# Kernel tuning notes

Hardware: AMD Instinct MI355X
Metric: run time of the kernel (lower is better)

The kernel has to match this reference:

```python
import jax, jax.numpy as jnp
import numpy as np

D_MODEL = 1024
D_STATE = 16
D_CONV = 4
LN_EPS = 1e-5


def setup_inputs() -> dict:
    key = jax.random.key(0)
    ks = jax.random.split(key, 12)
    B, T, D = 2, 2048, D_MODEL
    DI, DS, K = D_MODEL, D_STATE, D_CONV
    s = lambda k, shape, fan: jax.random.normal(k, shape, dtype=jnp.float32) * (1.0 / np.sqrt(fan))
    return {
        "x": jax.random.normal(ks[0], (B, T, D), dtype=jnp.float32),
        "ln_g": jnp.ones((D,), jnp.float32),
        "ln_b": jnp.zeros((D,), jnp.float32),
        "W_in": s(ks[1], (D, 2 * DI), D),          # x @ W_in -> [B,T,2*DI]
        "conv_w": s(ks[2], (DI, 1, K), K),          # depthwise conv kernel (OIH)
        "conv_b": jnp.zeros((DI,), jnp.float32),
        "dt_w": s(ks[3], (DI, DI), DI),
        "dt_b": jnp.zeros((DI,), jnp.float32),
        "B_w": s(ks[4], (DI, DS), DI),
        "C_w": s(ks[5], (DI, DS), DI),
        "log_A": jnp.log(jnp.linspace(1.0, 16.0, DI)).astype(jnp.float32),
        "D_param": jnp.ones((DI,), jnp.float32),
        "W_out": s(ks[6], (DI, D), DI),
    }


def _layernorm(x, g, b):
    mu = jnp.mean(x, axis=-1, keepdims=True)
    var = jnp.mean(jnp.square(x - mu), axis=-1, keepdims=True)
    return (x - mu) * jax.lax.rsqrt(var + LN_EPS) * g + b


def _causal_depthwise_conv(x, w, b):
    # x: [B,T,DI], w: [DI,1,K] -> causal conv, output [B,T,DI]
    xc = jnp.transpose(x, (0, 2, 1))  # [B,DI,T]
    K = w.shape[-1]
    out = jax.lax.conv_general_dilated(
        xc, w, window_strides=(1,), padding=[(K - 1, 0)],
        dimension_numbers=("NCH", "OIH", "NCH"),
        feature_group_count=x.shape[-1])
    return jnp.transpose(out, (0, 2, 1)) + b


def _ssm_scan(x, dt, Bm, Cm, A):
    # x, dt: [B,T,DI]; Bm, Cm: [B,T,DS]; A: [DI]
    Bsz, T, DI = x.shape
    DS = Bm.shape[-1]
    h0 = jnp.zeros((Bsz, DI, DS), jnp.float32)

    def step(h, inp):
        xt, dtt, bt, ct = inp  # [B,DI],[B,DI],[B,DS],[B,DS]
        decay = jnp.exp(jnp.minimum(dtt * A, 0.0))            # [B,DI]
        h = h * decay[..., None] + (dtt * xt)[..., None] * bt[:, None, :]
        y = jnp.einsum("bds,bs->bd", h, ct)
        return h, y

    xs = (jnp.swapaxes(x, 0, 1), jnp.swapaxes(dt, 0, 1),
          jnp.swapaxes(Bm, 0, 1), jnp.swapaxes(Cm, 0, 1))
    _, ys = jax.lax.scan(step, h0, xs)  # ys: [T,B,DI]
    return jnp.swapaxes(ys, 0, 1)


def reference(x, ln_g, ln_b, W_in, conv_w, conv_b, dt_w, dt_b, B_w, C_w, log_A, D_param, W_out):
    residual = x
    xn = _layernorm(x, ln_g, ln_b)
    xz = xn @ W_in                         # [B,T,2*DI]
    x_ssm, z = jnp.split(xz, 2, axis=-1)
    x_ssm = _causal_depthwise_conv(x_ssm, conv_w, conv_b)
    x_ssm = jax.nn.silu(x_ssm)
    dt = jax.nn.softplus(x_ssm @ dt_w + dt_b)   # [B,T,DI]
    Bm = x_ssm @ B_w                            # [B,T,DS]
    Cm = x_ssm @ C_w                            # [B,T,DS]
    A = -jnp.exp(log_A.astype(jnp.float32))     # [DI]
    y = _ssm_scan(x_ssm, dt, Bm, Cm, A)
    y = y + x_ssm * D_param
    y = y * jax.nn.silu(z)
    y = y @ W_out
    return residual + y
```

## Files before the change

### kernel.cpp

```cpp
#include <hip/hip_runtime.h>
#include <cstddef>

#define TSEQ 2048
#define NB   2
#define DM   1024
#define DST  16
#define ROWS (NB*TSEQ)
#define GCH  32
#define LCH  64
#define NDTBC 1152

typedef float  f32x4  __attribute__((ext_vector_type(4)));
typedef short  bf16x8 __attribute__((ext_vector_type(8)));
typedef unsigned short us4 __attribute__((ext_vector_type(4)));
typedef unsigned short u16;

__device__ __forceinline__ float u2f(unsigned short u) {
  return __uint_as_float(((unsigned)u) << 16);
}
__device__ __forceinline__ unsigned short bf16_rn(float x) {
  unsigned u = __float_as_uint(x);
  u += 0x7fff + ((u >> 16) & 1);
  return (unsigned short)(u >> 16);
}
__device__ __forceinline__ void split1(float x, u16& h, u16& l) {
  h = bf16_rn(x);
  l = bf16_rn(x - u2f(h));
}
__device__ __forceinline__ void split4(const float4& v, us4& h, us4& l) {
  u16 h0, h1, h2, h3, l0, l1, l2, l3;
  split1(v.x, h0, l0); split1(v.y, h1, l1);
  split1(v.z, h2, l2); split1(v.w, h3, l3);
  h = (us4){h0, h1, h2, h3};
  l = (us4){l0, l1, l2, l3};
}
__device__ __forceinline__ float softplus_f(float x) {
  return fmaxf(x, 0.0f) + log1pf(expf(-fabsf(x)));
}
__device__ __forceinline__ float silu_f(float x) {
  return x / (1.0f + expf(-x));
}
__device__ __forceinline__ void async16(const void* g, void* l) {
  __builtin_amdgcn_global_load_lds(
      (const __attribute__((address_space(1))) unsigned int*)g,
      (__attribute__((address_space(3))) unsigned int*)l, 16, 0, 0);
}
__device__ __forceinline__ float block_reduce_sum(float v, float* smem) {
#pragma unroll
  for (int off = 32; off > 0; off >>= 1) v += __shfl_down(v, off);
  int wid = threadIdx.x >> 6, lane = threadIdx.x & 63;
  if (lane == 0) smem[wid] = v;
  __syncthreads();
  float r = (smem[0] + smem[1]) + (smem[2] + smem[3]);
  __syncthreads();
  return r;
}

__global__ __launch_bounds__(256) void wsplit_t(const float* __restrict__ W,
    u16* __restrict__ Th, u16* __restrict__ Tl, int K, int N) {
  __shared__ float t[32][33];
  int k0 = blockIdx.y * 32, n0 = blockIdx.x * 32;
  int r = threadIdx.x >> 3, cq = (threadIdx.x & 7) * 4;
  float4 v = *(const float4*)&W[(size_t)(k0 + r) * N + n0 + cq];
  t[r][cq + 0] = v.x; t[r][cq + 1] = v.y; t[r][cq + 2] = v.z; t[r][cq + 3] = v.w;
  __syncthreads();
  int n = threadIdx.x >> 3, kq = (threadIdx.x & 7) * 4;
  float4 w4;
  w4.x = t[kq + 0][n]; w4.y = t[kq + 1][n]; w4.z = t[kq + 2][n]; w4.w = t[kq + 3][n];
  us4 h, l;
  split4(w4, h, l);
  size_t o = (size_t)(n0 + n) * K + k0 + kq;
  *(us4*)&Th[o] = h;
  *(us4*)&Tl[o] = l;
}

__global__ __launch_bounds__(256) void bc_prep(const float* __restrict__ Bw,
    const float* __restrict__ Cw, u16* __restrict__ Th, u16* __restrict__ Tl) {
  int n = DM + blockIdx.x;
  int k = threadIdx.x * 4;
  float4 v = {0.f, 0.f, 0.f, 0.f};
  if (n < DM + DST) {
    int s = n - DM;
    v.x = Bw[(k + 0) * DST + s]; v.y = Bw[(k + 1) * DST + s];
    v.z = Bw[(k + 2) * DST + s]; v.w = Bw[(k + 3) * DST + s];
  } else if (n < DM + 2 * DST) {
    int s = n - DM - DST;
    v.x = Cw[(k + 0) * DST + s]; v.y = Cw[(k + 1) * DST + s];
    v.z = Cw[(k + 2) * DST + s]; v.w = Cw[(k + 3) * DST + s];
  }
  us4 h, l;
  split4(v, h, l);
  size_t o = (size_t)n * DM + k;
  *(us4*)&Th[o] = h;
  *(us4*)&Tl[o] = l;
}

__global__ __launch_bounds__(256) void ln_kernel(const float* __restrict__ x,
    const float* __restrict__ g, const float* __restrict__ b,
    u16* __restrict__ xh, u16* __restrict__ xl) {
  __shared__ float smem[4];
  int r = blockIdx.x;
  size_t base = (size_t)r * DM + threadIdx.x * 4;
  float4 x4 = *(const float4*)&x[base];
  float s = block_reduce_sum(x4.x + x4.y + x4.z + x4.w, smem);
  float mu = s * (1.0f / DM);
  float d0 = x4.x - mu, d1 = x4.y - mu, d2 = x4.z - mu, d3 = x4.w - mu;
  float v = block_reduce_sum(d0*d0 + d1*d1 + d2*d2 + d3*d3, smem) * (1.0f / DM);
  float inv = rsqrtf(v + 1e-5f);
  float4 g4 = *(const float4*)&g[threadIdx.x * 4];
  float4 b4 = *(const float4*)&b[threadIdx.x * 4];
  float4 o;
  o.x = d0 * inv * g4.x + b4.x;
  o.y = d1 * inv * g4.y + b4.y;
  o.z = d2 * inv * g4.z + b4.z;
  o.w = d3 * inv * g4.w + b4.w;
  us4 h, l;
  split4(o, h, l);
  *(us4*)&xh[base] = h;
  *(us4*)&xl[base] = l;
}

#define LBUF 12288
template <int EPI>
__global__ __launch_bounds__(256) void gemm_mfma(
    const u16* __restrict__ Ah, const u16* __restrict__ Al,
    const u16* __restrict__ Bh, const u16* __restrict__ Bl,
    float* __restrict__ C, int M, int N, int Kd,
    const float* __restrict__ bias, const float* __restrict__ resid,
    float* __restrict__ C2, float* __restrict__ C3) {
  __shared__ __align__(16) u16 lds[2 * LBUF];
  int tid = threadIdx.x, wave = tid >> 6, lane = tid & 63;
  int m0 = blockIdx.y * 128, n0 = blockIdx.x * 64;
  int wm = (wave >> 1) * 64, wn = (wave & 1) * 32;

  const u16* gptr[6];
  int ldst[6];
#pragma unroll
  for (int r = 0; r < 6; ++r) {
    int c = r * 256 + tid;
    int kq = c & 3;
    const u16* base;
    int row;
    if (c < 512)       { base = Ah + (size_t)m0 * Kd; row = c >> 2; }
    else if (c < 1024) { base = Al + (size_t)m0 * Kd; row = (c - 512) >> 2; }
    else if (c < 1280) { base = Bh + (size_t)n0 * Kd; row = (c - 1024) >> 2; }
    else               { base = Bl + (size_t)n0 * Kd; row = (c - 1280) >> 2; }
    gptr[r] = base + (size_t)row * Kd + kq * 8;
    ldst[r] = c * 8;
  }

  f32x4 acc[4][2];
#pragma unroll
  for (int i = 0; i < 4; ++i)
#pragma unroll
    for (int j = 0; j < 2; ++j) acc[i][j] = (f32x4){0.f, 0.f, 0.f, 0.f};
  int fr = lane & 15, quad = lane >> 4;

#pragma unroll
  for (int r = 0; r < 6; ++r) async16(gptr[r], lds + ldst[r]);

  int nsteps = Kd / 32;
  for (int s = 0; s < nsteps; ++s) {
    int cur = (s & 1) * LBUF;
    __syncthreads();
    if (s + 1 < nsteps) {
      int ko = (s + 1) * 32;
      int nxt = ((s + 1) & 1) * LBUF;
#pragma unroll
      for (int r = 0; r < 6; ++r) async16(gptr[r] + ko, lds + nxt + ldst[r]);
    }
    const u16* sAh = lds + cur;
    const u16* sAl = lds + cur + 4096;
    const u16* sBh = lds + cur + 8192;
    const u16* sBl = lds + cur + 10240;
    bf16x8 afh[4], afl[4], bfh[2], bfl[2];
#pragma unroll
    for (int t = 0; t < 4; ++t) {
      int ro = (wm + t * 16 + fr) * 32 + quad * 8;
      afh[t] = *(const bf16x8*)&sAh[ro];
      afl[t] = *(const bf16x8*)&sAl[ro];
    }
#pragma unroll
    for (int t = 0; t < 2; ++t) {
      int co = (wn + t * 16 + fr) * 32 + quad * 8;
      bfh[t] = *(const bf16x8*)&sBh[co];
      bfl[t] = *(const bf16x8*)&sBl[co];
    }
#pragma unroll
    for (int mt = 0; mt < 4; ++mt)
#pragma unroll
      for (int nt = 0; nt < 2; ++nt) {
        acc[mt][nt] = __builtin_amdgcn_mfma_f32_16x16x32_bf16(afh[mt], bfh[nt], acc[mt][nt], 0, 0, 0);
        acc[mt][nt] = __builtin_amdgcn_mfma_f32_16x16x32_bf16(afh[mt], bfl[nt], acc[mt][nt], 0, 0, 0);
        acc[mt][nt] = __builtin_amdgcn_mfma_f32_16x16x32_bf16(afl[mt], bfh[nt], acc[mt][nt], 0, 0, 0);
      }
  }

#pragma unroll
  for (int mt = 0; mt < 4; ++mt)
#pragma unroll
    for (int nt = 0; nt < 2; ++nt) {
      int col = n0 + wn + nt * 16 + fr;
#pragma unroll
      for (int r = 0; r < 4; ++r) {
        int row = m0 + wm + mt * 16 + quad * 4 + r;
        float v = acc[mt][nt][r];
        if (EPI == 2) {
          v += resid[(size_t)row * N + col];
          C[(size_t)row * N + col] = v;
        } else if (EPI == 3) {
          if (col < DM) C[(size_t)row * DM + col] = v;
          else          C2[(size_t)row * DM + col - DM] = v;
        } else if (EPI == 4) {
          if (col < DM) {
            C[(size_t)row * DM + col] = softplus_f(v + bias[col]);
          } else if (col < DM + DST) {
            C2[(size_t)row * DST + col - DM] = v;
          } else if (col < DM + 2 * DST) {
            C3[(size_t)row * DST + col - DM - DST] = v;
          }
        } else {
          C[(size_t)row * N + col] = v;
        }
      }
    }
}

__global__ __launch_bounds__(256) void conv_silu_kernel(
    const float* __restrict__ xin, const float* __restrict__ w,
    const float* __restrict__ cb, u16* __restrict__ xsh, u16* __restrict__ xsl) {
  int r = blockIdx.x;
  int b = r >> 11, t = r & 2047;
  int d = threadIdx.x * 4;
  float4 w0 = *(const float4*)&w[(d + 0) * 4];
  float4 w1 = *(const float4*)&w[(d + 1) * 4];
  float4 w2 = *(const float4*)&w[(d + 2) * 4];
  float4 w3 = *(const float4*)&w[(d + 3) * 4];
  float4 s = *(const float4*)&cb[d];
#pragma unroll
  for (int k = 0; k < 4; ++k) {
    int ts = t + k - 3;
    if (ts >= 0) {
      float4 xv = *(const float4*)&xin[((size_t)(b * TSEQ + ts)) * DM + d];
      s.x = fmaf(xv.x, (&w0.x)[k], s.x);
      s.y = fmaf(xv.y, (&w1.x)[k], s.y);
      s.z = fmaf(xv.z, (&w2.x)[k], s.z);
      s.w = fmaf(xv.w, (&w3.x)[k], s.w);
    }
  }
  float4 o;
  o.x = silu_f(s.x); o.y = silu_f(s.y); o.z = silu_f(s.z); o.w = silu_f(s.w);
  us4 h, l;
  split4(o, h, l);
  size_t base = (size_t)r * DM + d;
  *(us4*)&xsh[base] = h;
  *(us4*)&xsl[base] = l;
}

__global__ __launch_bounds__(256) void scan_a_kernel(
    const float* __restrict__ dt, const u16* __restrict__ xsh,
    const u16* __restrict__ xsl,
    const float* __restrict__ Bm, const float* __restrict__ Cm,
    const float* __restrict__ logA, float* __restrict__ yloc,
    float* __restrict__ cumP, float* __restrict__ hend) {
  int blk = blockIdx.x;
  int dblk = blk & 3, c = (blk >> 2) & 31, b = blk >> 7;
  int di = dblk * 256 + threadIdx.x;
  __shared__ float sB[LCH][DST];
  __shared__ float sC[LCH][DST];
  {
    int tl = threadIdx.x >> 2, sq = (threadIdx.x & 3) * 4;
    size_t base = ((size_t)(b * TSEQ + c * LCH + tl)) * DST + sq;
    *(float4*)&sB[tl][sq] = *(const float4*)&Bm[base];
    *(float4*)&sC[tl][sq] = *(const float4*)&Cm[base];
  }
  __syncthreads();
  float A_di = -expf(logA[di]);
  float h[DST];
#pragma unroll
  for (int s = 0; s < DST; ++s) h[s] = 0.0f;
  float cp = 1.0f;
  for (int tl = 0; tl < LCH; ++tl) {
    size_t idx = ((size_t)(b * TSEQ + c * LCH + tl)) * DM + di;
    float dtv = dt[idx];
    float xv  = u2f(xsh[idx]) + u2f(xsl[idx]);
    float decay = expf(fminf(dtv * A_di, 0.0f));
    float u = dtv * xv;
    float y = 0.0f;
#pragma unroll
    for (int s4 = 0; s4 < 4; ++s4) {
      float4 b4 = *(const float4*)&sB[tl][s4 * 4];
      float4 c4 = *(const float4*)&sC[tl][s4 * 4];
      h[s4*4+0] = fmaf(h[s4*4+0], decay, u * b4.x); y = fmaf(h[s4*4+0], c4.x, y);
      h[s4*4+1] = fmaf(h[s4*4+1], decay, u * b4.y); y = fmaf(h[s4*4+1], c4.y, y);
      h[s4*4+2] = fmaf(h[s4*4+2], decay, u * b4.z); y = fmaf(h[s4*4+2], c4.z, y);
      h[s4*4+3] = fmaf(h[s4*4+3], decay, u * b4.w); y = fmaf(h[s4*4+3], c4.w, y);
    }
    cp *= decay;
    yloc[idx] = y;
    cumP[idx] = cp;
  }
#pragma unroll
  for (int s = 0; s < DST; ++s)
    hend[(((size_t)(b * GCH + c)) * DST + s) * DM + di] = h[s];
}

__global__ __launch_bounds__(256) void scan_b_kernel(
    const float* __restrict__ cumP, float* __restrict__ hboth) {
  int blk = blockIdx.x;
  int dblk = blk & 3, s = (blk >> 2) & 15, b = blk >> 6;
  int di = dblk * 256 + threadIdx.x;
  float H = 0.0f;
  for (int c = 0; c < GCH; ++c) {
    size_t hidx = (((size_t)(b * GCH + c)) * DST + s) * DM + di;
    float e = hboth[hidx];
    hboth[hidx] = H;
    float P = cumP[((size_t)(b * TSEQ + c * LCH + LCH - 1)) * DM + di];
    H = e + P * H;
  }
}

__global__ __launch_bounds__(256) void scan_c_kernel(
    const float* __restrict__ Cm, const float* __restrict__ Hinit,
    const u16* __restrict__ xsh, const u16* __restrict__ xsl,
    const float* __restrict__ zbuf,
    const float* __restrict__ Dp, const float* __restrict__ cumP,
    const float* __restrict__ yloc, u16* __restrict__ yh, u16* __restrict__ yl) {
  int r = blockIdx.x;
  int b = r >> 11, t = r & 2047, c = t >> 6;
  int di = threadIdx.x * 4;
  size_t idx = (size_t)r * DM + di;
  float4 y4 = *(const float4*)&yloc[idx];
  float4 p4 = *(const float4*)&cumP[idx];
  float4 dot = {0.f, 0.f, 0.f, 0.f};
  size_t hbase = ((size_t)(b * GCH + c)) * DST * DM + di;
#pragma unroll
  for (int s = 0; s < DST; ++s) {
    float cs = Cm[(size_t)r * DST + s];
    float4 h4 = *(const float4*)&Hinit[hbase + (size_t)s * DM];
    dot.x = fmaf(cs, h4.x, dot.x);
    dot.y = fmaf(cs, h4.y, dot.y);
    dot.z = fmaf(cs, h4.z, dot.z);
    dot.w = fmaf(cs, h4.w, dot.w);
  }
  y4.x = fmaf(p4.x, dot.x, y4.x);
  y4.y = fmaf(p4.y, dot.y, y4.y);
  y4.z = fmaf(p4.z, dot.z, y4.z);
  y4.w = fmaf(p4.w, dot.w, y4.w);
  us4 xh4 = *(const us4*)&xsh[idx];
  us4 xl4 = *(const us4*)&xsl[idx];
  float4 D4 = *(const float4*)&Dp[di];
  y4.x = fmaf(u2f(xh4.x) + u2f(xl4.x), D4.x, y4.x);
  y4.y = fmaf(u2f(xh4.y) + u2f(xl4.y), D4.y, y4.y);
  y4.z = fmaf(u2f(xh4.z) + u2f(xl4.z), D4.z, y4.z);
  y4.w = fmaf(u2f(xh4.w) + u2f(xl4.w), D4.w, y4.w);
  float4 z4 = *(const float4*)&zbuf[idx];
  y4.x *= silu_f(z4.x);
  y4.y *= silu_f(z4.y);
  y4.z *= silu_f(z4.z);
  y4.w *= silu_f(z4.w);
  us4 h, l;
  split4(y4, h, l);
  *(us4*)&yh[idx] = h;
  *(us4*)&yl[idx] = l;
}

extern "C" void kernel_launch(void* const* d_in, const int* in_sizes, int n_in,
                              void* d_out, int out_size, void* d_ws, size_t ws_size,
                              hipStream_t stream) {
  const float* x      = (const float*)d_in[0];
  const float* ln_g   = (const float*)d_in[1];
  const float* ln_b   = (const float*)d_in[2];
  const float* W_in   = (const float*)d_in[3];
  const float* conv_w = (const float*)d_in[4];
  const float* conv_b = (const float*)d_in[5];
  const float* dt_w   = (const float*)d_in[6];
  const float* dt_b   = (const float*)d_in[7];
  const float* B_w    = (const float*)d_in[8];
  const float* C_w    = (const float*)d_in[9];
  const float* log_A  = (const float*)d_in[10];
  const float* D_par  = (const float*)d_in[11];
  const float* W_out  = (const float*)d_in[12];
  float* out = (float*)d_out;

  float* ws = (float*)d_ws;
  const size_t NE = (size_t)ROWS * DM;
  float* bufX  = ws;
  float* bufZ  = bufX + NE;
  float* bufP  = bufZ + NE;
  float* bufY  = bufP + NE;
  u16*   actH  = (u16*)(bufY + NE);
  u16*   actL  = actH + NE;
  float* bufDT = (float*)(actH + 2 * NE);
  u16*   yH    = (u16*)bufDT;
  u16*   yL    = yH + NE;
  u16* winTh  = (u16*)bufP;
  u16* winTl  = winTh + (size_t)2 * DM * DM;
  u16* dtbcTh = winTl + (size_t)2 * DM * DM;
  u16* dtbcTl = dtbcTh + (size_t)NDTBC * DM;
  float* bufBm = bufX;
  float* bufCm = bufBm + (size_t)ROWS * DST;
  float* bufHe = bufCm + (size_t)ROWS * DST;
  u16* woutTh  = (u16*)(bufHe + (size_t)NB * GCH * DST * DM);
  u16* woutTl  = woutTh + (size_t)DM * DM;

  wsplit_t<<<dim3(2 * DM / 32, DM / 32), 256, 0, stream>>>(W_in, winTh, winTl, DM, 2 * DM);
  wsplit_t<<<dim3(DM / 32, DM / 32), 256, 0, stream>>>(dt_w, dtbcTh, dtbcTl, DM, DM);
  bc_prep<<<NDTBC - DM, 256, 0, stream>>>(B_w, C_w, dtbcTh, dtbcTl);
  ln_kernel<<<ROWS, 256, 0, stream>>>(x, ln_g, ln_b, actH, actL);
  gemm_mfma<3><<<dim3(2 * DM / 64, ROWS / 128), 256, 0, stream>>>(
      actH, actL, winTh, winTl, bufX, ROWS, 2 * DM, DM, nullptr, nullptr, bufZ, nullptr);
  conv_silu_kernel<<<ROWS, 256, 0, stream>>>(bufX, conv_w, conv_b, actH, actL);
  wsplit_t<<<dim3(DM / 32, DM / 32), 256, 0, stream>>>(W_out, woutTh, woutTl, DM, DM);
  gemm_mfma<4><<<dim3(NDTBC / 64, ROWS / 128), 256, 0, stream>>>(
      actH, actL, dtbcTh, dtbcTl, bufDT, ROWS, NDTBC, DM, dt_b, nullptr, bufBm, bufCm);
  scan_a_kernel<<<NB * GCH * 4, 256, 0, stream>>>(bufDT, actH, actL, bufBm, bufCm,
                                                  log_A, bufY, bufP, bufHe);
  scan_b_kernel<<<NB * DST * 4, 256, 0, stream>>>(bufP, bufHe);
  scan_c_kernel<<<ROWS, 256, 0, stream>>>(bufCm, bufHe, actH, actL, bufZ, D_par,
                                          bufP, bufY, yH, yL);
  gemm_mfma<2><<<dim3(DM / 64, ROWS / 128), 256, 0, stream>>>(
      yH, yL, woutTh, woutTl, out, ROWS, DM, DM, nullptr, x, nullptr, nullptr);
}
```

Before: 349.6 us.

## Restructure chunked scan into state-only pass and recompute pass with fused epilogue

```diff
diff --git a/kernel.cpp b/kernel.cpp
--- a/kernel.cpp
+++ b/kernel.cpp
@@ -257,12 +257,70 @@
   *(us4*)&xsl[base] = l;
 }
 
-__global__ __launch_bounds__(256) void scan_a_kernel(
+__global__ __launch_bounds__(256) void scan_pass1(
     const float* __restrict__ dt, const u16* __restrict__ xsh,
-    const u16* __restrict__ xsl,
-    const float* __restrict__ Bm, const float* __restrict__ Cm,
-    const float* __restrict__ logA, float* __restrict__ yloc,
-    float* __restrict__ cumP, float* __restrict__ hend) {
+    const u16* __restrict__ xsl, const float* __restrict__ Bm,
+    const float* __restrict__ logA,
+    float* __restrict__ hend, float* __restrict__ pend) {
+  int blk = blockIdx.x;
+  int dblk = blk & 3, c = (blk >> 2) & 31, b = blk >> 7;
+  int di = dblk * 256 + threadIdx.x;
+  __shared__ float sB[LCH][DST];
+  {
+    int tl = threadIdx.x >> 2, sq = (threadIdx.x & 3) * 4;
+    size_t base = ((size_t)(b * TSEQ + c * LCH + tl)) * DST + sq;
+    *(float4*)&sB[tl][sq] = *(const float4*)&Bm[base];
+  }
+  __syncthreads();
+  float A_di = -expf(logA[di]);
+  float h[DST];
+#pragma unroll
+  for (int s = 0; s < DST; ++s) h[s] = 0.0f;
+  float cp = 1.0f;
+  for (int tl = 0; tl < LCH; ++tl) {
+    size_t idx = ((size_t)(b * TSEQ + c * LCH + tl)) * DM + di;
+    float dtv = dt[idx];
+    float xv  = u2f(xsh[idx]) + u2f(xsl[idx]);
+    float decay = expf(fminf(dtv * A_di, 0.0f));
+    float u = dtv * xv;
+#pragma unroll
+    for (int s4 = 0; s4 < 4; ++s4) {
+      float4 b4 = *(const float4*)&sB[tl][s4 * 4];
+      h[s4*4+0] = fmaf(h[s4*4+0], decay, u * b4.x);
+      h[s4*4+1] = fmaf(h[s4*4+1], decay, u * b4.y);
+      h[s4*4+2] = fmaf(h[s4*4+2], decay, u * b4.z);
+      h[s4*4+3] = fmaf(h[s4*4+3], decay, u * b4.w);
+    }
+    cp *= decay;
+  }
+#pragma unroll
+  for (int s = 0; s < DST; ++s)
+    hend[(((size_t)(b * GCH + c)) * DST + s) * DM + di] = h[s];
+  pend[((size_t)(b * GCH + c)) * DM + di] = cp;
+}
+
+__global__ __launch_bounds__(256) void scan_b_kernel(
+    const float* __restrict__ pend, float* __restrict__ hboth) {
+  int blk = blockIdx.x;
+  int dblk = blk & 3, s = (blk >> 2) & 15, b = blk >> 6;
+  int di = dblk * 256 + threadIdx.x;
+  float H = 0.0f;
+  for (int c = 0; c < GCH; ++c) {
+    size_t hidx = (((size_t)(b * GCH + c)) * DST + s) * DM + di;
+    float e = hboth[hidx];
+    hboth[hidx] = H;
+    float P = pend[((size_t)(b * GCH + c)) * DM + di];
+    H = e + P * H;
+  }
+}
+
+__global__ __launch_bounds__(256) void scan_pass2(
+    const float* __restrict__ dt, const u16* __restrict__ xsh,
+    const u16* __restrict__ xsl, const float* __restrict__ Bm,
+    const float* __restrict__ Cm, const float* __restrict__ logA,
+    const float* __restrict__ Hinit, const float* __restrict__ Dp,
+    const float* __restrict__ zbuf,
+    u16* __restrict__ yh, u16* __restrict__ yl) {
   int blk = blockIdx.x;
   int dblk = blk & 3, c = (blk >> 2) & 31, b = blk >> 7;
   int di = dblk * 256 + threadIdx.x;
@@ -276,10 +334,11 @@
   }
   __syncthreads();
   float A_di = -expf(logA[di]);
+  float Dv = Dp[di];
   float h[DST];
-#pragma unroll
-  for (int s = 0; s < DST; ++s) h[s] = 0.0f;
-  float cp = 1.0f;
+  size_t hbase = ((size_t)(b * GCH + c)) * DST * DM + di;
+#pragma unroll
+  for (int s = 0; s < DST; ++s) h[s] = Hinit[hbase + (size_t)s * DM];
   for (int tl = 0; tl < LCH; ++tl) {
     size_t idx = ((size_t)(b * TSEQ + c * LCH + tl)) * DM + di;
     float dtv = dt[idx];
@@ -296,73 +355,13 @@
       h[s4*4+2] = fmaf(h[s4*4+2], decay, u * b4.z); y = fmaf(h[s4*4+2], c4.z, y);
       h[s4*4+3] = fmaf(h[s4*4+3], decay, u * b4.w); y = fmaf(h[s4*4+3], c4.w, y);
     }
-    cp *= decay;
-    yloc[idx] = y;
-    cumP[idx] = cp;
-  }
-#pragma unroll
-  for (int s = 0; s < DST; ++s)
-    hend[(((size_t)(b * GCH + c)) * DST + s) * DM + di] = h[s];
-}
-
-__global__ __launch_bounds__(256) void scan_b_kernel(
-    const float* __restrict__ cumP, float* __restrict__ hboth) {
-  int blk = blockIdx.x;
-  int dblk = blk & 3, s = (blk >> 2) & 15, b = blk >> 6;
-  int di = dblk * 256 + threadIdx.x;
-  float H = 0.0f;
-  for (int c = 0; c < GCH; ++c) {
-    size_t hidx = (((size_t)(b * GCH + c)) * DST + s) * DM + di;
-    float e = hboth[hidx];
-    hboth[hidx] = H;
-    float P = cumP[((size_t)(b * TSEQ + c * LCH + LCH - 1)) * DM + di];
-    H = e + P * H;
-  }
-}
-
-__global__ __launch_bounds__(256) void scan_c_kernel(
-    const float* __restrict__ Cm, const float* __restrict__ Hinit,
-    const u16* __restrict__ xsh, const u16* __restrict__ xsl,
-    const float* __restrict__ zbuf,
-    const float* __restrict__ Dp, const float* __restrict__ cumP,
-    const float* __restrict__ yloc, u16* __restrict__ yh, u16* __restrict__ yl) {
-  int r = blockIdx.x;
-  int b = r >> 11, t = r & 2047, c = t >> 6;
-  int di = threadIdx.x * 4;
-  size_t idx = (size_t)r * DM + di;
-  float4 y4 = *(const float4*)&yloc[idx];
-  float4 p4 = *(const float4*)&cumP[idx];
-  float4 dot = {0.f, 0.f, 0.f, 0.f};
-  size_t hbase = ((size_t)(b * GCH + c)) * DST * DM + di;
-#pragma unroll
-  for (int s = 0; s < DST; ++s) {
-    float cs = Cm[(size_t)r * DST + s];
-    float4 h4 = *(const float4*)&Hinit[hbase + (size_t)s * DM];
-    dot.x = fmaf(cs, h4.x, dot.x);
-    dot.y = fmaf(cs, h4.y, dot.y);
-    dot.z = fmaf(cs, h4.z, dot.z);
-    dot.w = fmaf(cs, h4.w, dot.w);
-  }
-  y4.x = fmaf(p4.x, dot.x, y4.x);
-  y4.y = fmaf(p4.y, dot.y, y4.y);
-  y4.z = fmaf(p4.z, dot.z, y4.z);
-  y4.w = fmaf(p4.w, dot.w, y4.w);
-  us4 xh4 = *(const us4*)&xsh[idx];
-  us4 xl4 = *(const us4*)&xsl[idx];
-  float4 D4 = *(const float4*)&Dp[di];
-  y4.x = fmaf(u2f(xh4.x) + u2f(xl4.x), D4.x, y4.x);
-  y4.y = fmaf(u2f(xh4.y) + u2f(xl4.y), D4.y, y4.y);
-  y4.z = fmaf(u2f(xh4.z) + u2f(xl4.z), D4.z, y4.z);
-  y4.w = fmaf(u2f(xh4.w) + u2f(xl4.w), D4.w, y4.w);
-  float4 z4 = *(const float4*)&zbuf[idx];
-  y4.x *= silu_f(z4.x);
-  y4.y *= silu_f(z4.y);
-  y4.z *= silu_f(z4.z);
-  y4.w *= silu_f(z4.w);
-  us4 h, l;
-  split4(y4, h, l);
-  *(us4*)&yh[idx] = h;
-  *(us4*)&yl[idx] = l;
+    y = fmaf(xv, Dv, y);
+    y *= silu_f(zbuf[idx]);
+    u16 hh, ll;
+    split1(y, hh, ll);
+    yh[idx] = hh;
+    yl[idx] = ll;
+  }
 }
 
 extern "C" void kernel_launch(void* const* d_in, const int* in_sizes, int n_in,
@@ -387,14 +386,15 @@
   const size_t NE = (size_t)ROWS * DM;
   float* bufX  = ws;
   float* bufZ  = bufX + NE;
-  float* bufP  = bufZ + NE;
-  float* bufY  = bufP + NE;
+  float* bufW  = bufZ + NE;
+  float* bufY  = bufW + NE;
   u16*   actH  = (u16*)(bufY + NE);
   u16*   actL  = actH + NE;
   float* bufDT = (float*)(actH + 2 * NE);
-  u16*   yH    = (u16*)bufDT;
+  u16*   yH    = (u16*)bufY;
   u16*   yL    = yH + NE;
-  u16* winTh  = (u16*)bufP;
+  float* bufPe = bufW;
+  u16* winTh  = (u16*)bufW;
   u16* winTl  = winTh + (size_t)2 * DM * DM;
   u16* dtbcTh = winTl + (size_t)2 * DM * DM;
   u16* dtbcTl = dtbcTh + (size_t)NDTBC * DM;
@@ -414,11 +414,11 @@
   wsplit_t<<<dim3(DM / 32, DM / 32), 256, 0, stream>>>(W_out, woutTh, woutTl, DM, DM);
   gemm_mfma<4><<<dim3(NDTBC / 64, ROWS / 128), 256, 0, stream>>>(
       actH, actL, dtbcTh, dtbcTl, bufDT, ROWS, NDTBC, DM, dt_b, nullptr, bufBm, bufCm);
-  scan_a_kernel<<<NB * GCH * 4, 256, 0, stream>>>(bufDT, actH, actL, bufBm, bufCm,
-                                                  log_A, bufY, bufP, bufHe);
-  scan_b_kernel<<<NB * DST * 4, 256, 0, stream>>>(bufP, bufHe);
-  scan_c_kernel<<<ROWS, 256, 0, stream>>>(bufCm, bufHe, actH, actL, bufZ, D_par,
-                                          bufP, bufY, yH, yL);
+  scan_pass1<<<NB * GCH * 4, 256, 0, stream>>>(bufDT, actH, actL, bufBm,
+                                               log_A, bufHe, bufPe);
+  scan_b_kernel<<<NB * DST * 4, 256, 0, stream>>>(bufPe, bufHe);
+  scan_pass2<<<NB * GCH * 4, 256, 0, stream>>>(bufDT, actH, actL, bufBm, bufCm,
+                                               log_A, bufHe, D_par, bufZ, yH, yL);
   gemm_mfma<2><<<dim3(DM / 64, ROWS / 128), 256, 0, stream>>>(
       yH, yL, woutTh, woutTl, out, ROWS, DM, DM, nullptr, x, nullptr, nullptr);
 }
```

After: 350.5 us. No clear change (+0.2%).
